# Performance work log

Measured on AMD Instinct MI355X. Metric: run time of the kernel, lower is better.

The kernel has to match this reference:

```python
import jax, jax.numpy as jnp
import numpy as np
from jax import lax

DIM = 128
HEADS = 4
B, H, W = 8, 128, 128


def conv1x1(x, w, b):
    # x: [B,C,H,W], w: [O,I,1,1]
    y = lax.conv_general_dilated(x, w, (1, 1), 'VALID',
                                 dimension_numbers=('NCHW', 'OIHW', 'NCHW'))
    return y + b[None, :, None, None]


def dwconv3x3(x, w, b):
    # depthwise: w: [C,1,3,3], groups=C
    C = x.shape[1]
    y = lax.conv_general_dilated(x, w, (1, 1), ((1, 1), (1, 1)),
                                 dimension_numbers=('NCHW', 'OIHW', 'NCHW'),
                                 feature_group_count=C)
    return y + b[None, :, None, None]


def setup_inputs() -> dict:
    key = jax.random.key(0)
    ks = jax.random.split(key, 7)
    s = 0.02
    return {
        'x': jax.random.normal(ks[0], (B, DIM, H, W), jnp.float32),
        'qkv_w': jax.random.normal(ks[1], (3 * DIM, DIM, 1, 1), jnp.float32) * s,
        'qkv_b': jnp.zeros((3 * DIM,), jnp.float32),
        'dw_w': jax.random.normal(ks[2], (3 * DIM, 1, 3, 3), jnp.float32) * s,
        'dw_b': jnp.zeros((3 * DIM,), jnp.float32),
        'proj_w': jax.random.normal(ks[3], (DIM, DIM, 1, 1), jnp.float32) * s,
        'proj_b': jnp.zeros((DIM,), jnp.float32),
        'temperature': jnp.ones((HEADS, 1, 1, 1), jnp.float32),
    }


def reference(x, qkv_w, qkv_b, dw_w, dw_b, proj_w, proj_b, temperature):
    b, C, h, w = x.shape
    heads = temperature.shape[0]
    c = C // heads

    qkv = dwconv3x3(conv1x1(x, qkv_w, qkv_b), dw_w, dw_b)
    q, k, v = jnp.split(qkv, 3, axis=1)

    # b (head c) h w -> b head c h w
    q = q.reshape(b, heads, c, h, w)
    k = k.reshape(b, heads, c, h, w)
    v = v.reshape(b, heads, c, h, w)

    # L2-normalize along H (axis=-2), matching torch F.normalize eps=1e-12
    eps = 1e-12
    q = q / jnp.maximum(jnp.linalg.norm(q, axis=-2, keepdims=True), eps)
    k = k / jnp.maximum(jnp.linalg.norm(k, axis=-2, keepdims=True), eps)

    # attn[b,n,c,j,k] = sum_i q[b,n,c,i,j] * k_[b,n,c,i,k]  -> [b,head,c,W,W]
    attn = jnp.einsum('bncij,bncik->bncjk', q, k) * temperature
    attn = jax.nn.softmax(attn, axis=-2)

    # out[b,n,c,i,k] = sum_j v[b,n,c,i,j] * attn[b,n,c,j,k]
    out = jnp.einsum('bncij,bncjk->bncik', v, attn)
    out = out.reshape(b, C, h, w)
    return conv1x1(out, proj_w, proj_b)
```

## Files before the change

### kernel.cpp

```cpp
#include <hip/hip_runtime.h>

typedef unsigned short u16;
typedef unsigned int   u32;

typedef short bf16x8 __attribute__((ext_vector_type(8)));
typedef float f32x4  __attribute__((ext_vector_type(4)));

__device__ __forceinline__ float bf2f(u16 u) { return __uint_as_float(((u32)u) << 16); }
__device__ __forceinline__ u16 f2bf(float f) {
    u32 u = __float_as_uint(f);
    return (u16)((u + 0x7fffu + ((u >> 16) & 1u)) >> 16);
}

#define MFMA16(a, b, c) __builtin_amdgcn_mfma_f32_16x16x32_bf16(a, b, c, 0, 0, 0)

__global__ __launch_bounds__(512, 1) void k_qkv(const float* __restrict__ x,
                                                const float* __restrict__ w,
                                                const float* __restrict__ bias,
                                                u16* __restrict__ out1) {
    extern __shared__ char smem[];
    u16* xT = (u16*)smem;
    u16* Cs = xT + 128 * 136;
    const int h = blockIdx.x, b = blockIdx.y;
    const int t = threadIdx.x;

    const float* xb = x + (((size_t)(b * 128)) << 14) + (h << 7);
    for (int it = 0; it < 32; ++it) {
        int idx = it * 512 + t;
        int ci = idx >> 7, p = idx & 127;
        xT[p * 136 + ci] = f2bf(xb[((size_t)ci << 14) + p]);
    }
    __syncthreads();

    const int wave = t >> 6, lane = t & 63, m16 = lane & 15, quad = lane >> 4;
    f32x4 acc[3][8] = {};
    for (int kk = 0; kk < 4; ++kk) {
        const int kb = kk * 32 + quad * 8;
        bf16x8 afr[3];
#pragma unroll
        for (int mt = 0; mt < 3; ++mt) {
            const float* wp = w + (wave * 48 + mt * 16 + m16) * 128 + kb;
            float4 w0 = *(const float4*)wp;
            float4 w1 = *(const float4*)(wp + 4);
            bf16x8 a;
            a[0] = (short)f2bf(w0.x); a[1] = (short)f2bf(w0.y);
            a[2] = (short)f2bf(w0.z); a[3] = (short)f2bf(w0.w);
            a[4] = (short)f2bf(w1.x); a[5] = (short)f2bf(w1.y);
            a[6] = (short)f2bf(w1.z); a[7] = (short)f2bf(w1.w);
            afr[mt] = a;
        }
#pragma unroll
        for (int nt = 0; nt < 8; ++nt) {
            bf16x8 bfr = *(const bf16x8*)(&xT[(nt * 16 + m16) * 136 + kb]);
            acc[0][nt] = MFMA16(afr[0], bfr, acc[0][nt]);
            acc[1][nt] = MFMA16(afr[1], bfr, acc[1][nt]);
            acc[2][nt] = MFMA16(afr[2], bfr, acc[2][nt]);
        }
    }
    float bco[3][4];
#pragma unroll
    for (int mt = 0; mt < 3; ++mt)
#pragma unroll
        for (int r = 0; r < 4; ++r) bco[mt][r] = bias[wave * 48 + mt * 16 + quad * 4 + r];
#pragma unroll
    for (int mt = 0; mt < 3; ++mt)
#pragma unroll
        for (int nt = 0; nt < 8; ++nt) {
            int p = nt * 16 + m16;
#pragma unroll
            for (int r = 0; r < 4; ++r)
                Cs[(wave * 48 + mt * 16 + quad * 4 + r) * 136 + p] = f2bf(acc[mt][nt][r] + bco[mt][r]);
        }
    __syncthreads();

    u16* ob = out1 + (((size_t)(b * 384)) << 14) + (h << 7);
    for (int it = 0; it < 12; ++it) {
        int idx = it * 512 + t;
        int co = idx >> 4, cp = idx & 15;
        *(uint4*)(&ob[((size_t)co << 14) + cp * 8]) = *(const uint4*)(&Cs[co * 136 + cp * 8]);
    }
}

__global__ __launch_bounds__(256, 4) void k_dw(const u16* __restrict__ in,
                                               const float* __restrict__ w,
                                               const float* __restrict__ bias,
                                               u16* __restrict__ out) {
    __shared__ u16 tile[34 * 144];
    const int htile = blockIdx.x;
    const int ch = blockIdx.y;
    const int b = blockIdx.z;
    const int t = threadIdx.x;
    const u16* base = in + (((size_t)(b * 384 + ch)) << 14);

    if (t < 68) {
        int r = t >> 1, side = t & 1;
        uint4 z = {0, 0, 0, 0};
        *(uint4*)(&tile[r * 144 + side * 136]) = z;
    }
    for (int it = 0; it < 3; ++it) {
        int idx = it * 256 + t;
        if (idx < 544) {
            int r = idx >> 4, cq = idx & 15;
            int y = htile * 32 - 1 + r;
            uint4 v = {0, 0, 0, 0};
            if (y >= 0 && y <= 127) v = *(const uint4*)(base + (y << 7) + cq * 8);
            *(uint4*)(&tile[r * 144 + 8 + cq * 8]) = v;
        }
    }
    float wg[9];
#pragma unroll
    for (int i = 0; i < 9; ++i) wg[i] = w[ch * 9 + i];
    const float bv = bias[ch];
    __syncthreads();

    const int r = t >> 4, cp = t & 15, c0 = cp * 8;
    u16* ob = out + (((size_t)(b * 384 + ch)) << 14) + ((htile * 32) << 7) + c0;
#pragma unroll
    for (int half = 0; half < 2; ++half) {
        const int ro = r + half * 16;
        float acc[8];
#pragma unroll
        for (int c = 0; c < 8; ++c) acc[c] = bv;
#pragma unroll
        for (int dy = 0; dy < 3; ++dy) {
            const u16* row = &tile[(ro + dy) * 144 + 8 + c0];
            float v[10];
            v[0] = bf2f(row[-1]);
            uint4 m = *(const uint4*)row;
            v[1] = bf2f((u16)(m.x & 0xffff)); v[2] = bf2f((u16)(m.x >> 16));
            v[3] = bf2f((u16)(m.y & 0xffff)); v[4] = bf2f((u16)(m.y >> 16));
            v[5] = bf2f((u16)(m.z & 0xffff)); v[6] = bf2f((u16)(m.z >> 16));
            v[7] = bf2f((u16)(m.w & 0xffff)); v[8] = bf2f((u16)(m.w >> 16));
            v[9] = bf2f(row[8]);
#pragma unroll
            for (int dx = 0; dx < 3; ++dx) {
                const float wv = wg[dy * 3 + dx];
#pragma unroll
                for (int c = 0; c < 8; ++c) acc[c] += wv * v[c + dx];
            }
        }
        u32 pk[4];
#pragma unroll
        for (int c2 = 0; c2 < 4; ++c2) {
            u32 lo = f2bf(acc[2 * c2]), hi = f2bf(acc[2 * c2 + 1]);
            pk[c2] = lo | (hi << 16);
        }
        *(uint4*)(ob + (ro << 7)) = *(uint4*)pk;
    }
}

__global__ __launch_bounds__(512, 1) void k_attn(const u16* __restrict__ qkv,
                                                 const float* __restrict__ temp,
                                                 u16* __restrict__ outp) {
    extern __shared__ char smem[];
    u16* Qt = (u16*)smem;
    u16* Kt = Qt + 128 * 136;
    u16* Vs = Kt + 128 * 136;
    u16* Pt = Vs + 128 * 136;
    float* rq = (float*)(Pt + 128 * 136);
    float* rk = rq + 128;
    float* St = (float*)smem;
    u16* Osh = (u16*)smem;

    const int ch = blockIdx.x, b = blockIdx.y;
    const int head = ch >> 5;
    const int t = threadIdx.x;
    const size_t qoff = ((size_t)(b * 384 + ch)) << 14;
    const size_t koff = ((size_t)(b * 384 + 128 + ch)) << 14;
    const size_t voff = ((size_t)(b * 384 + 256 + ch)) << 14;

    for (int it = 0; it < 4; ++it) {
        int idx = it * 512 + t;
        int row = idx >> 4, cp = idx & 15;
        *(uint4*)(&Vs[row * 136 + cp * 8]) = *(const uint4*)(&qkv[voff + (row << 7) + cp * 8]);
    }
    for (int it = 0; it < 32; ++it) {
        int idx = it * 512 + t;
        int i = idx >> 7, j = idx & 127;
        Qt[j * 136 + i] = qkv[qoff + (i << 7) + j];
        Kt[j * 136 + i] = qkv[koff + (i << 7) + j];
    }
    __syncthreads();

    if (t < 256) {
        const u16* rowp = (t < 128) ? &Qt[t * 136] : &Kt[(t - 128) * 136];
        float s = 0.f;
#pragma unroll
        for (int c = 0; c < 16; ++c) {
            uint4 v = *(const uint4*)(rowp + c * 8);
            float f0 = bf2f((u16)(v.x & 0xffff)), f1 = bf2f((u16)(v.x >> 16));
            float f2 = bf2f((u16)(v.y & 0xffff)), f3 = bf2f((u16)(v.y >> 16));
            float f4 = bf2f((u16)(v.z & 0xffff)), f5 = bf2f((u16)(v.z >> 16));
            float f6 = bf2f((u16)(v.w & 0xffff)), f7 = bf2f((u16)(v.w >> 16));
            s += f0 * f0 + f1 * f1 + f2 * f2 + f3 * f3 + f4 * f4 + f5 * f5 + f6 * f6 + f7 * f7;
        }
        float r = 1.0f / fmaxf(sqrtf(s), 1e-12f);
        if (t < 128) rq[t] = r; else rk[t - 128] = r;
    }
    __syncthreads();

    const int wave = t >> 6, lane = t & 63, m16 = lane & 15, quad = lane >> 4;

    f32x4 acc[8] = {};
    for (int kk = 0; kk < 4; ++kk) {
        const int kb = kk * 32 + quad * 8;
        bf16x8 a = *(const bf16x8*)(&Qt[(wave * 16 + m16) * 136 + kb]);
#pragma unroll
        for (int nt = 0; nt < 8; ++nt) {
            bf16x8 bf = *(const bf16x8*)(&Kt[(nt * 16 + m16) * 136 + kb]);
            acc[nt] = MFMA16(a, bf, acc[nt]);
        }
    }
    const float tv = temp[head];
    float rqv[4];
#pragma unroll
    for (int r = 0; r < 4; ++r) rqv[r] = rq[wave * 16 + quad * 4 + r] * tv;
    __syncthreads();
#pragma unroll
    for (int nt = 0; nt < 8; ++nt) {
        int kcol = nt * 16 + m16;
        float rkv = rk[kcol];
        f32x4 v = acc[nt], o;
        o[0] = v[0] * rqv[0] * rkv; o[1] = v[1] * rqv[1] * rkv;
        o[2] = v[2] * rqv[2] * rkv; o[3] = v[3] * rqv[3] * rkv;
        *(f32x4*)(&St[kcol * 132 + wave * 16 + quad * 4]) = o;
    }
    __syncthreads();

    {
        const int col = t >> 2, part = t & 3;
        const float* Srow = &St[col * 132 + part * 32];
        float e[32];
#pragma unroll
        for (int c = 0; c < 8; ++c) {
            f32x4 v = *(const f32x4*)(&Srow[c * 4]);
            e[c * 4 + 0] = v[0]; e[c * 4 + 1] = v[1]; e[c * 4 + 2] = v[2]; e[c * 4 + 3] = v[3];
        }
        float lmax = -1e30f;
#pragma unroll
        for (int jj = 0; jj < 32; ++jj) lmax = fmaxf(lmax, e[jj]);
        lmax = fmaxf(lmax, __shfl_xor(lmax, 1));
        lmax = fmaxf(lmax, __shfl_xor(lmax, 2));
        float lsum = 0.f;
#pragma unroll
        for (int jj = 0; jj < 32; ++jj) { e[jj] = __expf(e[jj] - lmax); lsum += e[jj]; }
        lsum += __shfl_xor(lsum, 1);
        lsum += __shfl_xor(lsum, 2);
        float inv = 1.0f / lsum;
        u32* prow = (u32*)&Pt[col * 136 + part * 32];
#pragma unroll
        for (int c2 = 0; c2 < 16; ++c2) {
            u32 lo = f2bf(e[2 * c2] * inv), hi = f2bf(e[2 * c2 + 1] * inv);
            prow[c2] = lo | (hi << 16);
        }
    }
    __syncthreads();

    f32x4 acc2[8] = {};
    for (int kk = 0; kk < 4; ++kk) {
        const int kb = kk * 32 + quad * 8;
        bf16x8 a = *(const bf16x8*)(&Vs[(wave * 16 + m16) * 136 + kb]);
#pragma unroll
        for (int nt = 0; nt < 8; ++nt) {
            bf16x8 bf = *(const bf16x8*)(&Pt[(nt * 16 + m16) * 136 + kb]);
            acc2[nt] = MFMA16(a, bf, acc2[nt]);
        }
    }
#pragma unroll
    for (int nt = 0; nt < 8; ++nt) {
        int kcol = nt * 16 + m16;
#pragma unroll
        for (int r = 0; r < 4; ++r)
            Osh[(wave * 16 + quad * 4 + r) * 136 + kcol] = f2bf(acc2[nt][r]);
    }
    __syncthreads();

    u16* ob = outp + (((size_t)(b * 128 + ch)) << 14);
    for (int it = 0; it < 4; ++it) {
        int idx = it * 512 + t;
        int row = idx >> 4, cp = idx & 15;
        *(uint4*)(&ob[(row << 7) + cp * 8]) = *(const uint4*)(&Osh[row * 136 + cp * 8]);
    }
}

__global__ __launch_bounds__(512, 1) void k_proj(const u16* __restrict__ ain,
                                                 const float* __restrict__ w,
                                                 const float* __restrict__ bias,
                                                 float* __restrict__ outp) {
    extern __shared__ char smem[];
    u16* xT = (u16*)smem;
    float* Cs = (float*)(xT + 128 * 136);
    const int h = blockIdx.x, b = blockIdx.y;
    const int t = threadIdx.x;

    const u16* ab = ain + (((size_t)(b * 128)) << 14) + (h << 7);
    for (int it = 0; it < 32; ++it) {
        int idx = it * 512 + t;
        int ci = idx >> 7, p = idx & 127;
        xT[p * 136 + ci] = ab[((size_t)ci << 14) + p];
    }
    __syncthreads();

    const int wave = t >> 6, lane = t & 63, m16 = lane & 15, quad = lane >> 4;
    f32x4 acc[8] = {};
    for (int kk = 0; kk < 4; ++kk) {
        const int kb = kk * 32 + quad * 8;
        const float* wp = w + (wave * 16 + m16) * 128 + kb;
        float4 w0 = *(const float4*)wp;
        float4 w1 = *(const float4*)(wp + 4);
        bf16x8 a;
        a[0] = (short)f2bf(w0.x); a[1] = (short)f2bf(w0.y);
        a[2] = (short)f2bf(w0.z); a[3] = (short)f2bf(w0.w);
        a[4] = (short)f2bf(w1.x); a[5] = (short)f2bf(w1.y);
        a[6] = (short)f2bf(w1.z); a[7] = (short)f2bf(w1.w);
#pragma unroll
        for (int nt = 0; nt < 8; ++nt) {
            bf16x8 bf = *(const bf16x8*)(&xT[(nt * 16 + m16) * 136 + kb]);
            acc[nt] = MFMA16(a, bf, acc[nt]);
        }
    }
    float bv[4];
#pragma unroll
    for (int r = 0; r < 4; ++r) bv[r] = bias[wave * 16 + quad * 4 + r];
#pragma unroll
    for (int nt = 0; nt < 8; ++nt) {
        int p = nt * 16 + m16;
#pragma unroll
        for (int r = 0; r < 4; ++r)
            Cs[(wave * 16 + quad * 4 + r) * 132 + p] = acc[nt][r] + bv[r];
    }
    __syncthreads();

    float* ob = outp + (((size_t)(b * 128)) << 14) + (h << 7);
    for (int it = 0; it < 8; ++it) {
        int idx = it * 512 + t;
        int row = idx >> 5, cp = idx & 31;
        *(float4*)(&ob[((size_t)row << 14) + cp * 4]) = *(const float4*)(&Cs[row * 132 + cp * 4]);
    }
}

extern "C" void kernel_launch(void* const* d_in, const int* in_sizes, int n_in,
                              void* d_out, int out_size, void* d_ws, size_t ws_size,
                              hipStream_t stream) {
    const float* x      = (const float*)d_in[0];
    const float* qkv_w  = (const float*)d_in[1];
    const float* qkv_b  = (const float*)d_in[2];
    const float* dw_w   = (const float*)d_in[3];
    const float* dw_b   = (const float*)d_in[4];
    const float* proj_w = (const float*)d_in[5];
    const float* proj_b = (const float*)d_in[6];
    const float* temp   = (const float*)d_in[7];
    float* out = (float*)d_out;

    u16* buf1 = (u16*)d_ws;
    u16* buf2 = buf1 + (size_t)8 * 384 * 16384;

    hipFuncSetAttribute((const void*)k_qkv,  hipFuncAttributeMaxDynamicSharedMemorySize, 139264);
    hipFuncSetAttribute((const void*)k_attn, hipFuncAttributeMaxDynamicSharedMemorySize, 140288);
    hipFuncSetAttribute((const void*)k_proj, hipFuncAttributeMaxDynamicSharedMemorySize, 102400);

    k_qkv<<<dim3(128, 8), 512, 139264, stream>>>(x, qkv_w, qkv_b, buf1);
    k_dw<<<dim3(4, 384, 8), 256, 0, stream>>>(buf1, dw_w, dw_b, buf2);
    k_attn<<<dim3(128, 8), 512, 140288, stream>>>(buf2, temp, buf1);
    k_proj<<<dim3(128, 8), 512, 102400, stream>>>(buf1, proj_w, proj_b, out);
}
```

Measured before the change: 279.5 us.

## Split QKV projection into bf16 transpose pre-pass and channel-grouped GEMM

```diff
diff --git a/kernel.cpp b/kernel.cpp
--- a/kernel.cpp
+++ b/kernel.cpp
@@ -14,67 +14,103 @@
 
 #define MFMA16(a, b, c) __builtin_amdgcn_mfma_f32_16x16x32_bf16(a, b, c, 0, 0, 0)
 
-__global__ __launch_bounds__(512, 1) void k_qkv(const float* __restrict__ x,
+__global__ __launch_bounds__(256, 4) void k_xpose(const float* __restrict__ x,
+                                                  u16* __restrict__ xT) {
+    __shared__ u16 Xs[128 * 128];
+    const int ptile = blockIdx.x, b = blockIdx.y;
+    const int t = threadIdx.x;
+    const float* xb = x + (((size_t)b) << 21) + ptile * 128;
+#pragma unroll
+    for (int i = 0; i < 16; ++i) {
+        int idx = i * 256 + t;
+        int ci = idx >> 5, pq = idx & 31;
+        float4 v = *(const float4*)(xb + (((size_t)ci) << 14) + pq * 4);
+        u32 lo = (u32)f2bf(v.x) | ((u32)f2bf(v.y) << 16);
+        u32 hi = (u32)f2bf(v.z) | ((u32)f2bf(v.w) << 16);
+        uint2 pk; pk.x = lo; pk.y = hi;
+        int cq = ci >> 3;
+        *(uint2*)(&Xs[ci * 128 + ((pq ^ cq) << 2)]) = pk;
+    }
+    __syncthreads();
+    u16* ob = xT + (((size_t)b) << 21) + ((size_t)(ptile * 128)) * 128;
+#pragma unroll
+    for (int j = 0; j < 8; ++j) {
+        int p = j * 16 + (t >> 4), cq = t & 15;
+        u16 tmp[8];
+#pragma unroll
+        for (int c = 0; c < 8; ++c) {
+            int ci = cq * 8 + c;
+            tmp[c] = Xs[ci * 128 + (((p >> 2) ^ cq) << 2) + (p & 3)];
+        }
+        *(uint4*)(&ob[(size_t)p * 128 + cq * 8]) = *(const uint4*)tmp;
+    }
+}
+
+__global__ __launch_bounds__(512, 2) void k_qkv(const u16* __restrict__ xT,
                                                 const float* __restrict__ w,
                                                 const float* __restrict__ bias,
                                                 u16* __restrict__ out1) {
     extern __shared__ char smem[];
-    u16* xT = (u16*)smem;
-    u16* Cs = xT + 128 * 136;
-    const int h = blockIdx.x, b = blockIdx.y;
+    u16* Bt = (u16*)smem;
+    u16* Cs = Bt + 2048 * 8;
+    const int h = blockIdx.x, cg = blockIdx.y, b = blockIdx.z;
     const int t = threadIdx.x;
 
-    const float* xb = x + (((size_t)(b * 128)) << 14) + (h << 7);
-    for (int it = 0; it < 32; ++it) {
-        int idx = it * 512 + t;
-        int ci = idx >> 7, p = idx & 127;
-        xT[p * 136 + ci] = f2bf(xb[((size_t)ci << 14) + p]);
-    }
-    __syncthreads();
+    const u16* xb = xT + (((size_t)b) << 21) + ((size_t)(h * 128)) * 128;
+#pragma unroll
+    for (int i = 0; i < 4; ++i) {
+        int slot = i * 512 + t;
+        int p = slot >> 4, g = slot & 15;
+        int gg = g ^ (p & 15);
+        uint4 v = *(const uint4*)(&xb[p * 128 + gg * 8]);
+        *(uint4*)(&Bt[slot * 8]) = v;
+    }
 
     const int wave = t >> 6, lane = t & 63, m16 = lane & 15, quad = lane >> 4;
-    f32x4 acc[3][8] = {};
-    for (int kk = 0; kk < 4; ++kk) {
-        const int kb = kk * 32 + quad * 8;
-        bf16x8 afr[3];
-#pragma unroll
-        for (int mt = 0; mt < 3; ++mt) {
-            const float* wp = w + (wave * 48 + mt * 16 + m16) * 128 + kb;
-            float4 w0 = *(const float4*)wp;
-            float4 w1 = *(const float4*)(wp + 4);
+    bf16x8 afr[4];
+    {
+        const float* wp0 = w + (size_t)(cg * 128 + wave * 16 + m16) * 128 + quad * 8;
+#pragma unroll
+        for (int kk = 0; kk < 4; ++kk) {
+            float4 w0 = *(const float4*)(wp0 + kk * 32);
+            float4 w1 = *(const float4*)(wp0 + kk * 32 + 4);
             bf16x8 a;
             a[0] = (short)f2bf(w0.x); a[1] = (short)f2bf(w0.y);
             a[2] = (short)f2bf(w0.z); a[3] = (short)f2bf(w0.w);
             a[4] = (short)f2bf(w1.x); a[5] = (short)f2bf(w1.y);
             a[6] = (short)f2bf(w1.z); a[7] = (short)f2bf(w1.w);
-            afr[mt] = a;
-        }
-#pragma unroll
-        for (int nt = 0; nt < 8; ++nt) {
-            bf16x8 bfr = *(const bf16x8*)(&xT[(nt * 16 + m16) * 136 + kb]);
-            acc[0][nt] = MFMA16(afr[0], bfr, acc[0][nt]);
-            acc[1][nt] = MFMA16(afr[1], bfr, acc[1][nt]);
-            acc[2][nt] = MFMA16(afr[2], bfr, acc[2][nt]);
-        }
-    }
-    float bco[3][4];
-#pragma unroll
-    for (int mt = 0; mt < 3; ++mt)
-#pragma unroll
-        for (int r = 0; r < 4; ++r) bco[mt][r] = bias[wave * 48 + mt * 16 + quad * 4 + r];
-#pragma unroll
-    for (int mt = 0; mt < 3; ++mt)
+            afr[kk] = a;
+        }
+    }
+    __syncthreads();
+
+    f32x4 acc[8] = {};
+#pragma unroll
+    for (int kk = 0; kk < 4; ++kk) {
+        const int g = kk * 4 + quad;
 #pragma unroll
         for (int nt = 0; nt < 8; ++nt) {
             int p = nt * 16 + m16;
-#pragma unroll
-            for (int r = 0; r < 4; ++r)
-                Cs[(wave * 48 + mt * 16 + quad * 4 + r) * 136 + p] = f2bf(acc[mt][nt][r] + bco[mt][r]);
-        }
-    __syncthreads();
-
-    u16* ob = out1 + (((size_t)(b * 384)) << 14) + (h << 7);
-    for (int it = 0; it < 12; ++it) {
+            bf16x8 bf = *(const bf16x8*)(&Bt[p * 128 + ((g ^ (p & 15)) << 3)]);
+            acc[nt] = MFMA16(afr[kk], bf, acc[nt]);
+        }
+    }
+
+    float bv[4];
+#pragma unroll
+    for (int r = 0; r < 4; ++r) bv[r] = bias[cg * 128 + wave * 16 + quad * 4 + r];
+#pragma unroll
+    for (int nt = 0; nt < 8; ++nt) {
+        int p = nt * 16 + m16;
+#pragma unroll
+        for (int r = 0; r < 4; ++r)
+            Cs[(wave * 16 + quad * 4 + r) * 136 + p] = f2bf(acc[nt][r] + bv[r]);
+    }
+    __syncthreads();
+
+    u16* ob = out1 + (((size_t)(b * 384 + cg * 128)) << 14) + (h << 7);
+#pragma unroll
+    for (int it = 0; it < 4; ++it) {
         int idx = it * 512 + t;
         int co = idx >> 4, cp = idx & 15;
         *(uint4*)(&ob[((size_t)co << 14) + cp * 8]) = *(const uint4*)(&Cs[co * 136 + cp * 8]);
@@ -355,11 +391,12 @@
     u16* buf1 = (u16*)d_ws;
     u16* buf2 = buf1 + (size_t)8 * 384 * 16384;
 
-    hipFuncSetAttribute((const void*)k_qkv,  hipFuncAttributeMaxDynamicSharedMemorySize, 139264);
+    hipFuncSetAttribute((const void*)k_qkv,  hipFuncAttributeMaxDynamicSharedMemorySize, 67584);
     hipFuncSetAttribute((const void*)k_attn, hipFuncAttributeMaxDynamicSharedMemorySize, 140288);
     hipFuncSetAttribute((const void*)k_proj, hipFuncAttributeMaxDynamicSharedMemorySize, 102400);
 
-    k_qkv<<<dim3(128, 8), 512, 139264, stream>>>(x, qkv_w, qkv_b, buf1);
+    k_xpose<<<dim3(128, 8), 256, 0, stream>>>(x, buf2);
+    k_qkv<<<dim3(128, 3, 8), 512, 67584, stream>>>(buf2, qkv_w, qkv_b, buf1);
     k_dw<<<dim3(4, 384, 8), 256, 0, stream>>>(buf1, dw_w, dw_b, buf2);
     k_attn<<<dim3(128, 8), 512, 140288, stream>>>(buf2, temp, buf1);
     k_proj<<<dim3(128, 8), 512, 102400, stream>>>(buf1, proj_w, proj_b, out);
```

Result: faster. 271.0 us (-3.1%).
